# Kernel optimization log

Measured on AMD Instinct MI355X. Metric: run time of the kernel, lower is better.

## Reference

```python
import jax, jax.numpy as jnp
import numpy as np

B, D, E, K = 16384, 1024, 8, 2  # tokens, embed_size, experts, top-k
W_IMPORTANCE = 0.01


def setup_inputs() -> dict:
    key = jax.random.key(0)
    ks = jax.random.split(key, 8)
    s = 1.0 / np.sqrt(D)
    return {
        "x": jax.random.normal(ks[0], (B, D), dtype=jnp.float32),   # fused vision features
        "q": jax.random.normal(ks[1], (B, D), dtype=jnp.float32),   # text features
        # cross-attention (seq_len=1) collapses to V then output projection
        "Wv": jax.random.normal(ks[2], (D, D), dtype=jnp.float32) * s,
        "bv": jnp.zeros((D,), dtype=jnp.float32),
        "Wo": jax.random.normal(ks[3], (D, D), dtype=jnp.float32) * s,
        "bo": jnp.zeros((D,), dtype=jnp.float32),
        # gate linear
        "Wg": jax.random.normal(ks[4], (D, E), dtype=jnp.float32) * s,
        "bg": jnp.zeros((E,), dtype=jnp.float32),
        # experts: Linear -> SiLU -> Linear
        "W1": jax.random.normal(ks[5], (E, D, D), dtype=jnp.float32) * s,
        "b1": jnp.zeros((E, D), dtype=jnp.float32),
        "W2": jax.random.normal(ks[6], (E, D, D), dtype=jnp.float32) * s,
        "b2": jnp.zeros((E, D), dtype=jnp.float32),
    }


def reference(x, q, Wv, bv, Wo, bo, Wg, bg, W1, b1, W2, b2):
    # CrossAttention with q_len = kv_len = 1: softmax over a single key is 1,
    # so attention output = out_proj(V(q)).
    att = (q @ Wv + bv) @ Wo + bo                      # (B, D)
    gate_logits = att @ Wg + bg                        # (B, E)
    gate_prob = jax.nn.softmax(gate_logits, axis=-1)   # eval mode: no noise
    top_w, top_i = jax.lax.top_k(gate_prob, K)         # (B, K)
    top_w = jax.nn.softmax(top_w, axis=-1)             # renormalize over top-k

    y = jnp.zeros_like(x)
    for e in range(E):  # small fixed expert count
        w_e = jnp.sum(jnp.where(top_i == e, top_w, 0.0), axis=-1)  # (B,)
        h = jax.nn.silu(x @ W1[e] + b1[e]) @ W2[e] + b2[e]         # (B, D)
        y = y + w_e[:, None] * h

    importance = gate_prob.sum(axis=0)  # (E,)
    importance_loss = W_IMPORTANCE * (jnp.std(importance, ddof=1) / jnp.mean(importance)) ** 2
    return y, gate_prob, importance_loss
```

## Files before the change

kernel.cpp:

```cpp
#include <hip/hip_runtime.h>
#include <hip/hip_bf16.h>

#define Btok 16384
#define Ddim 1024
#define Eexp 8

typedef __attribute__((ext_vector_type(8))) short short8;
typedef __attribute__((ext_vector_type(4))) float f32x4;

__device__ inline unsigned short f2bf(float f) {
    unsigned int u = __float_as_uint(f);
    unsigned int r = (u + 0x7fffu + ((u >> 16) & 1u)) >> 16;
    return (unsigned short)r;
}

__device__ inline void gload16(const void* g, void* l) {
    __builtin_amdgcn_global_load_lds(
        (const __attribute__((address_space(1))) void*)g,
        (__attribute__((address_space(3))) void*)l, 16, 0, 0);
}

__global__ __launch_bounds__(256) void k_tmp(const float* __restrict__ Wo,
                                             const float* __restrict__ Wg,
                                             float* __restrict__ tmp) {
    int id = blockIdx.x * 256 + threadIdx.x;
    int d = id >> 3, e = id & 7;
    double s = 0.0;
    for (int k = 0; k < Ddim; ++k)
        s += (double)Wo[(long)d * Ddim + k] * (double)Wg[k * Eexp + e];
    tmp[id] = (float)s;
}

__global__ __launch_bounds__(256) void k_wc(const float* __restrict__ Wv,
                                            const float* __restrict__ tmp,
                                            float* __restrict__ WcT) {
    int id = blockIdx.x * 256 + threadIdx.x;
    int d = id >> 3, e = id & 7;
    double s = 0.0;
    for (int k = 0; k < Ddim; ++k)
        s += (double)Wv[(long)d * Ddim + k] * (double)tmp[k * Eexp + e];
    WcT[e * Ddim + d] = (float)s;
}

__global__ __launch_bounds__(512) void k_bc(const float* __restrict__ bv,
                                            const float* __restrict__ bo,
                                            const float* __restrict__ bg,
                                            const float* __restrict__ Wg,
                                            const float* __restrict__ tmp,
                                            float* __restrict__ bcomb) {
    int w = threadIdx.x >> 6, l = threadIdx.x & 63;
    double s = 0.0;
    for (int k = l; k < Ddim; k += 64)
        s += (double)bv[k] * (double)tmp[k * Eexp + w] +
             (double)bo[k] * (double)Wg[k * Eexp + w];
    #pragma unroll
    for (int off = 32; off; off >>= 1) s += __shfl_xor(s, off);
    if (l == 0) bcomb[w] = (float)s + bg[w];
}

__global__ __launch_bounds__(256) void k_convx(const float4* __restrict__ x,
                                               ushort4* __restrict__ xb) {
    int i = blockIdx.x * 256 + threadIdx.x;
    float4 v = x[i];
    ushort4 o;
    o.x = f2bf(v.x); o.y = f2bf(v.y); o.z = f2bf(v.z); o.w = f2bf(v.w);
    xb[i] = o;
}

__global__ __launch_bounds__(256) void k_convw(const float* __restrict__ W1,
                                               const float* __restrict__ W2,
                                               unsigned short* __restrict__ w1bT,
                                               unsigned short* __restrict__ w2bT) {
    __shared__ float tile[32][33];
    int bid = blockIdx.x;
    int arr = bid >> 13;
    int e = (bid >> 10) & 7, bi = (bid >> 5) & 31, bj = bid & 31;
    const float* src = (arr ? W2 : W1) + (long)e * Ddim * Ddim;
    unsigned short* dst = (arr ? w2bT : w1bT) + (long)e * Ddim * Ddim;
    int tr = threadIdx.x >> 5, tc = threadIdx.x & 31;
    #pragma unroll
    for (int i = 0; i < 4; ++i) {
        int dl = tr + i * 8;
        tile[dl][tc] = src[(long)(bi * 32 + dl) * Ddim + bj * 32 + tc];
    }
    __syncthreads();
    #pragma unroll
    for (int i = 0; i < 4; ++i) {
        int nl = tr + i * 8;
        dst[(long)(bj * 32 + nl) * Ddim + bi * 32 + tc] = f2bf(tile[tc][nl]);
    }
}

__global__ __launch_bounds__(256) void k_gate(const float* __restrict__ q,
                                              const float* __restrict__ WcT,
                                              const float* __restrict__ bcomb,
                                              float* __restrict__ gate_prob,
                                              int* __restrict__ choice,
                                              float2* __restrict__ w12,
                                              float* __restrict__ impP) {
    __shared__ float impL[4][8];
    int w = threadIdx.x >> 6, l = threadIdx.x & 63;
    int t = blockIdx.x * 4 + w;
    const float* qr = q + (long)t * Ddim;
    float acc[8] = {0, 0, 0, 0, 0, 0, 0, 0};
    #pragma unroll
    for (int i = 0; i < 4; ++i) {
        float4 qv = *(const float4*)(qr + (i * 64 + l) * 4);
        #pragma unroll
        for (int e = 0; e < 8; ++e) {
            float4 wv = *(const float4*)(WcT + e * Ddim + (i * 64 + l) * 4);
            acc[e] += qv.x * wv.x + qv.y * wv.y + qv.z * wv.z + qv.w * wv.w;
        }
    }
    #pragma unroll
    for (int off = 32; off; off >>= 1)
        #pragma unroll
        for (int e = 0; e < 8; ++e) acc[e] += __shfl_xor(acc[e], off);
    float lg[8], p[8];
    float m = -1e30f;
    #pragma unroll
    for (int e = 0; e < 8; ++e) { lg[e] = acc[e] + bcomb[e]; m = fmaxf(m, lg[e]); }
    float s = 0.f;
    #pragma unroll
    for (int e = 0; e < 8; ++e) { p[e] = expf(lg[e] - m); s += p[e]; }
    float inv = 1.f / s;
    #pragma unroll
    for (int e = 0; e < 8; ++e) p[e] *= inv;
    float p1 = -1.f, p2 = -1.f; int i1 = 0, i2 = 0;
    #pragma unroll
    for (int e = 0; e < 8; ++e) {
        float pe = p[e];
        if (pe > p1) { p2 = p1; i2 = i1; p1 = pe; i1 = e; }
        else if (pe > p2) { p2 = pe; i2 = e; }
    }
    float ee = expf(p2 - p1);
    float wa = 1.f / (1.f + ee);
    float wb = ee / (1.f + ee);
    if (l == 0) {
        #pragma unroll
        for (int e = 0; e < 8; ++e) gate_prob[(long)t * 8 + e] = p[e];
        #pragma unroll
        for (int e = 0; e < 8; ++e) impL[w][e] = p[e];
        choice[t] = i1 | (i2 << 8);
        w12[t] = make_float2(wa, wb);
    }
    __syncthreads();
    if (threadIdx.x < 8)
        impP[blockIdx.x * 8 + threadIdx.x] =
            impL[0][threadIdx.x] + impL[1][threadIdx.x] +
            impL[2][threadIdx.x] + impL[3][threadIdx.x];
}

__global__ __launch_bounds__(256) void k_route(const int* __restrict__ choice,
                                               const float2* __restrict__ w12,
                                               int* __restrict__ counts,
                                               int* __restrict__ tok,
                                               float* __restrict__ wgt) {
    __shared__ int cnt[8];
    __shared__ int base[8];
    if (threadIdx.x < 8) cnt[threadIdx.x] = 0;
    __syncthreads();
    int t = blockIdx.x * 256 + threadIdx.x;
    int ch = choice[t];
    int i1 = ch & 255, i2 = ch >> 8;
    float2 ww = w12[t];
    int lp1 = atomicAdd(&cnt[i1], 1);
    int lp2 = atomicAdd(&cnt[i2], 1);
    __syncthreads();
    if (threadIdx.x < 8)
        base[threadIdx.x] = atomicAdd(&counts[threadIdx.x], cnt[threadIdx.x]);
    __syncthreads();
    int p1 = base[i1] + lp1;
    tok[i1 * Btok + p1] = t; wgt[i1 * Btok + p1] = ww.x;
    int p2 = base[i2] + lp2;
    tok[i2 * Btok + p2] = t; wgt[i2 * Btok + p2] = ww.y;
}

template <int MODE>
__global__ __launch_bounds__(512) void k_gemm(const unsigned short* __restrict__ Abase,
                                              const unsigned short* __restrict__ WT,
                                              const float* __restrict__ bias,
                                              const int* __restrict__ counts,
                                              const int* __restrict__ tok,
                                              const float* __restrict__ wgt,
                                              unsigned short* __restrict__ Hout,
                                              float* __restrict__ y) {
    __shared__ __align__(16) char lds[131072];

    int bid = blockIdx.x;
    int wg = (bid & 7) * 256 + (bid >> 3);
    int ct = wg & 3, rt = (wg >> 2) & 63, e = wg >> 8;

    int n_e = counts[e];
    int r0 = rt * 256;
    if (r0 >= n_e) return;
    int off_e = 0;
    #pragma unroll
    for (int j = 0; j < 8; ++j) off_e += (j < e) ? counts[j] : 0;
    int n0 = ct * 256;

    int t = threadIdx.x;
    int w = t >> 6, l = t & 63;
    int wm = w >> 2, wn = w & 3;

    int tr = t >> 3;
    int sc = (t & 7) ^ (tr & 7);
    const char* srcA[4]; const char* srcB[4];
    #pragma unroll
    for (int ri = 0; ri < 4; ++ri) {
        int idx = r0 + ri * 64 + tr; if (idx > n_e - 1) idx = n_e - 1;
        long g = (MODE == 0) ? (long)tok[e * Btok + idx] : (long)(off_e + idx);
        srcA[ri] = (const char*)Abase + g * 2048 + sc * 16;
        srcB[ri] = (const char*)WT + ((long)e << 21) + (long)(n0 + ri * 64 + tr) * 2048 + sc * 16;
    }

    int rowAb = (wm * 128 + (l & 15)) * 128;
    int rowBb = (wn * 64 + (l & 15)) * 128;
    int x0 = (((l >> 4)) ^ (l & 7)) << 4;
    int x1 = (((l >> 4) + 4) ^ (l & 7)) << 4;

    f32x4 acc[8][4];
    #pragma unroll
    for (int mi = 0; mi < 8; ++mi)
        #pragma unroll
        for (int ni = 0; ni < 4; ++ni) acc[mi][ni] = {0.f, 0.f, 0.f, 0.f};

    auto stage = [&](int b) {
        char* ab = (char*)lds + b * 32768;
        char* bb = (char*)lds + 65536 + b * 32768;
        #pragma unroll
        for (int ri = 0; ri < 4; ++ri) {
            gload16(srcA[ri], ab + ri * 8192 + w * 1024);
            gload16(srcB[ri], bb + ri * 8192 + w * 1024);
            srcA[ri] += 128; srcB[ri] += 128;
        }
    };

    const int NT = Ddim / 64;
    stage(0);
    __syncthreads();
    int buf = 0;
    for (int kk = 0; kk < NT; ++kk) {
        if (kk + 1 < NT) stage(buf ^ 1);
        const char* Ap = (const char*)lds + buf * 32768;
        const char* Bp = (const char*)lds + 65536 + buf * 32768;
        #pragma unroll
        for (int ks = 0; ks < 2; ++ks) {
            int xo = ks ? x1 : x0;
            short8 av[8], bv[4];
            #pragma unroll
            for (int mi = 0; mi < 8; ++mi)
                av[mi] = *(const short8*)(Ap + rowAb + mi * 2048 + xo);
            #pragma unroll
            for (int ni = 0; ni < 4; ++ni)
                bv[ni] = *(const short8*)(Bp + rowBb + ni * 2048 + xo);
            #pragma unroll
            for (int mi = 0; mi < 8; ++mi)
                #pragma unroll
                for (int ni = 0; ni < 4; ++ni)
                    acc[mi][ni] = __builtin_amdgcn_mfma_f32_16x16x32_bf16(av[mi], bv[ni], acc[mi][ni], 0, 0, 0);
        }
        __syncthreads();
        buf ^= 1;
    }

    float bias4[4];
    #pragma unroll
    for (int ni = 0; ni < 4; ++ni)
        bias4[ni] = bias[e * Ddim + n0 + wn * 64 + ni * 16 + (l & 15)];

    #pragma unroll
    for (int mi = 0; mi < 8; ++mi) {
        #pragma unroll
        for (int j = 0; j < 4; ++j) {
            int rl = wm * 128 + mi * 16 + (l >> 4) * 4 + j;
            int r = r0 + rl;
            bool ok = r < n_e;
            int trow = 0; float wr = 0.f;
            if (MODE == 1) {
                int ri = ok ? r : 0;
                trow = tok[e * Btok + ri];
                wr = wgt[e * Btok + ri];
            }
            #pragma unroll
            for (int ni = 0; ni < 4; ++ni) {
                int col = n0 + wn * 64 + ni * 16 + (l & 15);
                float v = acc[mi][ni][j] + bias4[ni];
                if (MODE == 0) {
                    v = v / (1.f + __expf(-v));
                    if (ok) Hout[(long)(off_e + r) * Ddim + col] = f2bf(v);
                } else {
                    if (ok) atomicAdd(&y[(long)trow * Ddim + col], wr * v);
                }
            }
        }
    }
}

__global__ __launch_bounds__(256) void k_loss(const float* __restrict__ impP,
                                              float* __restrict__ out) {
    __shared__ float red[256];
    __shared__ float impF[8];
    for (int e = 0; e < 8; ++e) {
        float s = 0.f;
        for (int i = threadIdx.x; i < 4096; i += 256) s += impP[i * 8 + e];
        red[threadIdx.x] = s;
        __syncthreads();
        for (int st = 128; st > 0; st >>= 1) {
            if ((int)threadIdx.x < st) red[threadIdx.x] += red[threadIdx.x + st];
            __syncthreads();
        }
        if (threadIdx.x == 0) impF[e] = red[0];
        __syncthreads();
    }
    if (threadIdx.x == 0) {
        double mean = 0.0;
        for (int e = 0; e < 8; ++e) mean += (double)impF[e];
        mean /= 8.0;
        double var = 0.0;
        for (int e = 0; e < 8; ++e) {
            double d = (double)impF[e] - mean;
            var += d * d;
        }
        var /= 7.0;
        out[0] = (float)(0.01 * var / (mean * mean));
    }
}

extern "C" void kernel_launch(void* const* d_in, const int* in_sizes, int n_in,
                              void* d_out, int out_size, void* d_ws, size_t ws_size,
                              hipStream_t stream) {
    const float* x  = (const float*)d_in[0];
    const float* q  = (const float*)d_in[1];
    const float* Wv = (const float*)d_in[2];
    const float* bv = (const float*)d_in[3];
    const float* Wo = (const float*)d_in[4];
    const float* bo = (const float*)d_in[5];
    const float* Wg = (const float*)d_in[6];
    const float* bg = (const float*)d_in[7];
    const float* W1 = (const float*)d_in[8];
    const float* b1 = (const float*)d_in[9];
    const float* W2 = (const float*)d_in[10];
    const float* b2 = (const float*)d_in[11];

    float* y = (float*)d_out;
    float* gate_prob = y + (long)Btok * Ddim;
    float* loss = gate_prob + (long)Btok * Eexp;

    char* ws = (char*)d_ws;
    int*   counts = (int*)(ws + 0);
    float* bcomb  = (float*)(ws + 256);
    float* tmp    = (float*)(ws + 512);
    float* WcT    = (float*)(ws + 33280);
    float* impP   = (float*)(ws + 66048);
    int*   choice = (int*)(ws + 197120);
    float2* w12   = (float2*)(ws + 262656);
    int*   tok    = (int*)(ws + 393728);
    float* wgt    = (float*)(ws + 918016);
    unsigned short* xb   = (unsigned short*)(ws + 1442304);
    unsigned short* w1bT = (unsigned short*)(ws + 34996736);
    unsigned short* w2bT = (unsigned short*)(ws + 51773952);
    unsigned short* H    = (unsigned short*)(ws + 68551168);

    hipMemsetAsync(counts, 0, 32, stream);
    hipMemsetAsync(y, 0, (size_t)Btok * Ddim * sizeof(float), stream);

    k_tmp<<<32, 256, 0, stream>>>(Wo, Wg, tmp);
    k_wc <<<32, 256, 0, stream>>>(Wv, tmp, WcT);
    k_bc <<<1, 512, 0, stream>>>(bv, bo, bg, Wg, tmp, bcomb);
    k_convx<<<16384, 256, 0, stream>>>((const float4*)x, (ushort4*)xb);
    k_convw<<<16384, 256, 0, stream>>>(W1, W2, w1bT, w2bT);
    k_gate<<<4096, 256, 0, stream>>>(q, WcT, bcomb, gate_prob, choice, w12, impP);
    k_route<<<64, 256, 0, stream>>>(choice, w12, counts, tok, wgt);
    k_gemm<0><<<2048, 512, 0, stream>>>(xb, w1bT, b1, counts, tok, wgt, H, nullptr);
    k_gemm<1><<<2048, 512, 0, stream>>>(H, w2bT, b2, counts, tok, wgt, nullptr, y);
    k_loss<<<1, 256, 0, stream>>>(impP, loss);
}
```

Measured before the change: 507.4 us.

## Restructure expert GEMM into quadrant-interleaved pipeline with explicit waitcnt and barriers

```diff
diff --git a/kernel.cpp b/kernel.cpp
--- a/kernel.cpp
+++ b/kernel.cpp
@@ -19,6 +19,11 @@
         (const __attribute__((address_space(1))) void*)g,
         (__attribute__((address_space(3))) void*)l, 16, 0, 0);
 }
+
+#define MEMF() asm volatile("" ::: "memory")
+#define BARRIER() do { MEMF(); __builtin_amdgcn_s_barrier(); MEMF(); } while (0)
+#define VMW(n) do { asm volatile("s_waitcnt vmcnt(" #n ")" ::: "memory"); \
+                    __builtin_amdgcn_sched_barrier(0); } while (0)
 
 __global__ __launch_bounds__(256) void k_tmp(const float* __restrict__ Wo,
                                              const float* __restrict__ Wg,
@@ -186,6 +191,7 @@
                                               unsigned short* __restrict__ Hout,
                                               float* __restrict__ y) {
     __shared__ __align__(16) char lds[131072];
+    char* ldsp = (char*)lds;
 
     int bid = blockIdx.x;
     int wg = (bid & 7) * 256 + (bid >> 3);
@@ -201,7 +207,7 @@
 
     int t = threadIdx.x;
     int w = t >> 6, l = t & 63;
-    int wm = w >> 2, wn = w & 3;
+    int wqm = w >> 1, wqn = w & 1;
 
     int tr = t >> 3;
     int sc = (t & 7) ^ (tr & 7);
@@ -213,88 +219,144 @@
         srcA[ri] = (const char*)Abase + g * 2048 + sc * 16;
         srcB[ri] = (const char*)WT + ((long)e << 21) + (long)(n0 + ri * 64 + tr) * 2048 + sc * 16;
     }
-
-    int rowAb = (wm * 128 + (l & 15)) * 128;
-    int rowBb = (wn * 64 + (l & 15)) * 128;
-    int x0 = (((l >> 4)) ^ (l & 7)) << 4;
+    int dstoff = tr * 128 + (t & 7) * 16;
+
+    int rA = (wqm * 32 + (l & 15)) * 128;
+    int rB = (wqn * 64 + (l & 15)) * 128;
+    int x0 = ((l >> 4) ^ (l & 7)) << 4;
     int x1 = (((l >> 4) + 4) ^ (l & 7)) << 4;
 
-    f32x4 acc[8][4];
-    #pragma unroll
-    for (int mi = 0; mi < 8; ++mi)
-        #pragma unroll
-        for (int ni = 0; ni < 4; ++ni) acc[mi][ni] = {0.f, 0.f, 0.f, 0.f};
-
-    auto stage = [&](int b) {
-        char* ab = (char*)lds + b * 32768;
-        char* bb = (char*)lds + 65536 + b * 32768;
-        #pragma unroll
-        for (int ri = 0; ri < 4; ++ri) {
-            gload16(srcA[ri], ab + ri * 8192 + w * 1024);
-            gload16(srcB[ri], bb + ri * 8192 + w * 1024);
-            srcA[ri] += 128; srcB[ri] += 128;
-        }
-    };
+    f32x4 acc[2][2][2][4];
+    #pragma unroll
+    for (int qa = 0; qa < 2; ++qa)
+        #pragma unroll
+        for (int qb = 0; qb < 2; ++qb)
+            #pragma unroll
+            for (int mi = 0; mi < 2; ++mi)
+                #pragma unroll
+                for (int ni = 0; ni < 4; ++ni) acc[qa][qb][mi][ni] = {0.f, 0.f, 0.f, 0.f};
+
+    short8 av[2][2], bv[4][2];
+
+#define STAGE_A(h, nb) do { \
+        char* d_ = ldsp + (nb) * 32768 + (h) * 16384 + dstoff; \
+        gload16(srcA[2*(h)], d_); gload16(srcA[2*(h)+1], d_ + 8192); \
+        srcA[2*(h)] += 128; srcA[2*(h)+1] += 128; } while (0)
+#define STAGE_B(h, nb) do { \
+        char* d_ = ldsp + 65536 + (nb) * 32768 + (h) * 16384 + dstoff; \
+        gload16(srcB[2*(h)], d_); gload16(srcB[2*(h)+1], d_ + 8192); \
+        srcB[2*(h)] += 128; srcB[2*(h)+1] += 128; } while (0)
+#define READ_AV(qa, c) do { \
+        const char* p_ = ldsp + (c) * 32768 + (qa) * 16384 + rA; \
+        av[0][0] = *(const short8*)(p_ + x0);        av[0][1] = *(const short8*)(p_ + x1); \
+        av[1][0] = *(const short8*)(p_ + 2048 + x0); av[1][1] = *(const short8*)(p_ + 2048 + x1); } while (0)
+#define READ_BV(qb, c) do { \
+        const char* p_ = ldsp + 65536 + (c) * 32768 + (qb) * 16384 + rB; \
+        _Pragma("unroll") \
+        for (int ni_ = 0; ni_ < 4; ++ni_) { \
+            bv[ni_][0] = *(const short8*)(p_ + ni_ * 2048 + x0); \
+            bv[ni_][1] = *(const short8*)(p_ + ni_ * 2048 + x1); } } while (0)
+#define MFMA16(qa, qb) do { \
+        __builtin_amdgcn_s_setprio(1); \
+        _Pragma("unroll") \
+        for (int mi_ = 0; mi_ < 2; ++mi_) \
+            _Pragma("unroll") \
+            for (int ni_ = 0; ni_ < 4; ++ni_) { \
+                acc[qa][qb][mi_][ni_] = __builtin_amdgcn_mfma_f32_16x16x32_bf16(av[mi_][0], bv[ni_][0], acc[qa][qb][mi_][ni_], 0, 0, 0); \
+                acc[qa][qb][mi_][ni_] = __builtin_amdgcn_mfma_f32_16x16x32_bf16(av[mi_][1], bv[ni_][1], acc[qa][qb][mi_][ni_], 0, 0, 0); } \
+        __builtin_amdgcn_s_setprio(0); \
+        __builtin_amdgcn_sched_barrier(0); } while (0)
 
     const int NT = Ddim / 64;
-    stage(0);
-    __syncthreads();
-    int buf = 0;
-    for (int kk = 0; kk < NT; ++kk) {
-        if (kk + 1 < NT) stage(buf ^ 1);
-        const char* Ap = (const char*)lds + buf * 32768;
-        const char* Bp = (const char*)lds + 65536 + buf * 32768;
-        #pragma unroll
-        for (int ks = 0; ks < 2; ++ks) {
-            int xo = ks ? x1 : x0;
-            short8 av[8], bv[4];
+    STAGE_A(0, 0); STAGE_B(0, 0); STAGE_A(1, 0); STAGE_B(1, 0);
+    VMW(4); BARRIER();
+
+    for (int kt = 0; kt < NT - 1; ++kt) {
+        int c = kt & 1, nb = c ^ 1;
+        READ_AV(0, c); READ_BV(0, c);
+        STAGE_A(0, nb);
+        BARRIER();
+        MFMA16(0, 0);
+        VMW(4); BARRIER();
+        READ_AV(1, c);
+        STAGE_B(0, nb);
+        BARRIER();
+        MFMA16(1, 0);
+        VMW(4); BARRIER();
+        READ_BV(1, c);
+        STAGE_A(1, nb);
+        BARRIER();
+        MFMA16(1, 1);
+        BARRIER();
+        READ_AV(0, c);
+        STAGE_B(1, nb);
+        BARRIER();
+        MFMA16(0, 1);
+        VMW(4); BARRIER();
+    }
+    {
+        const int c = (NT - 1) & 1;
+        READ_AV(0, c); READ_BV(0, c);
+        BARRIER();
+        MFMA16(0, 0);
+        VMW(2); BARRIER();
+        READ_AV(1, c);
+        BARRIER();
+        MFMA16(1, 0);
+        VMW(0); BARRIER();
+        READ_BV(1, c);
+        BARRIER();
+        MFMA16(1, 1);
+        BARRIER();
+        READ_AV(0, c);
+        BARRIER();
+        MFMA16(0, 1);
+    }
+
+    float bias8[2][4];
+    #pragma unroll
+    for (int qb = 0; qb < 2; ++qb)
+        #pragma unroll
+        for (int ni = 0; ni < 4; ++ni)
+            bias8[qb][ni] = bias[e * Ddim + n0 + qb * 128 + wqn * 64 + ni * 16 + (l & 15)];
+
+    #pragma unroll
+    for (int qa = 0; qa < 2; ++qa) {
+        #pragma unroll
+        for (int mi = 0; mi < 2; ++mi) {
             #pragma unroll
-            for (int mi = 0; mi < 8; ++mi)
-                av[mi] = *(const short8*)(Ap + rowAb + mi * 2048 + xo);
-            #pragma unroll
-            for (int ni = 0; ni < 4; ++ni)
-                bv[ni] = *(const short8*)(Bp + rowBb + ni * 2048 + xo);
-            #pragma unroll
-            for (int mi = 0; mi < 8; ++mi)
+            for (int j = 0; j < 4; ++j) {
+                int rl = qa * 128 + wqm * 32 + mi * 16 + (l >> 4) * 4 + j;
+                int r = r0 + rl;
+                bool ok = r < n_e;
+                int trow = 0; float wr = 0.f;
+                if (MODE == 1) {
+                    int ri = ok ? r : 0;
+                    trow = tok[e * Btok + ri];
+                    wr = wgt[e * Btok + ri];
+                }
                 #pragma unroll
-                for (int ni = 0; ni < 4; ++ni)
-                    acc[mi][ni] = __builtin_amdgcn_mfma_f32_16x16x32_bf16(av[mi], bv[ni], acc[mi][ni], 0, 0, 0);
-        }
-        __syncthreads();
-        buf ^= 1;
-    }
-
-    float bias4[4];
-    #pragma unroll
-    for (int ni = 0; ni < 4; ++ni)
-        bias4[ni] = bias[e * Ddim + n0 + wn * 64 + ni * 16 + (l & 15)];
-
-    #pragma unroll
-    for (int mi = 0; mi < 8; ++mi) {
-        #pragma unroll
-        for (int j = 0; j < 4; ++j) {
-            int rl = wm * 128 + mi * 16 + (l >> 4) * 4 + j;
-            int r = r0 + rl;
-            bool ok = r < n_e;
-            int trow = 0; float wr = 0.f;
-            if (MODE == 1) {
-                int ri = ok ? r : 0;
-                trow = tok[e * Btok + ri];
-                wr = wgt[e * Btok + ri];
-            }
-            #pragma unroll
-            for (int ni = 0; ni < 4; ++ni) {
-                int col = n0 + wn * 64 + ni * 16 + (l & 15);
-                float v = acc[mi][ni][j] + bias4[ni];
-                if (MODE == 0) {
-                    v = v / (1.f + __expf(-v));
-                    if (ok) Hout[(long)(off_e + r) * Ddim + col] = f2bf(v);
-                } else {
-                    if (ok) atomicAdd(&y[(long)trow * Ddim + col], wr * v);
+                for (int qb = 0; qb < 2; ++qb) {
+                    #pragma unroll
+                    for (int ni = 0; ni < 4; ++ni) {
+                        int col = n0 + qb * 128 + wqn * 64 + ni * 16 + (l & 15);
+                        float v = acc[qa][qb][mi][ni][j] + bias8[qb][ni];
+                        if (MODE == 0) {
+                            v = v / (1.f + __expf(-v));
+                            if (ok) Hout[(long)(off_e + r) * Ddim + col] = f2bf(v);
+                        } else {
+                            if (ok) atomicAdd(&y[(long)trow * Ddim + col], wr * v);
+                        }
+                    }
                 }
             }
         }
     }
+#undef STAGE_A
+#undef STAGE_B
+#undef READ_AV
+#undef READ_BV
+#undef MFMA16
 }
 
 __global__ __launch_bounds__(256) void k_loss(const float* __restrict__ impP,
```

Measured after the change: 510.9 us. About the same (+0.7%).

## Shrink expert GEMM tiles to 128x128 with 256 threads and single-buffered LDS

Applied to the files above, without the earlier changes.

```diff
diff --git a/kernel.cpp b/kernel.cpp
--- a/kernel.cpp
+++ b/kernel.cpp
@@ -177,91 +177,83 @@
 }
 
 template <int MODE>
-__global__ __launch_bounds__(512) void k_gemm(const unsigned short* __restrict__ Abase,
-                                              const unsigned short* __restrict__ WT,
-                                              const float* __restrict__ bias,
-                                              const int* __restrict__ counts,
-                                              const int* __restrict__ tok,
-                                              const float* __restrict__ wgt,
-                                              unsigned short* __restrict__ Hout,
-                                              float* __restrict__ y) {
-    __shared__ __align__(16) char lds[131072];
+__global__ __launch_bounds__(256, 4) void k_gemm(const unsigned short* __restrict__ Abase,
+                                                 const unsigned short* __restrict__ WT,
+                                                 const float* __restrict__ bias,
+                                                 const int* __restrict__ counts,
+                                                 const int* __restrict__ tok,
+                                                 const float* __restrict__ wgt,
+                                                 unsigned short* __restrict__ Hout,
+                                                 float* __restrict__ y) {
+    __shared__ __align__(16) char lds[32768];
+    char* ldsp = (char*)lds;
 
     int bid = blockIdx.x;
-    int wg = (bid & 7) * 256 + (bid >> 3);
-    int ct = wg & 3, rt = (wg >> 2) & 63, e = wg >> 8;
+    int e = bid & 7;
+    int k = bid >> 3;
+    int rt = k >> 3, ct = k & 7;
 
     int n_e = counts[e];
-    int r0 = rt * 256;
+    int r0 = rt * 128;
     if (r0 >= n_e) return;
     int off_e = 0;
     #pragma unroll
     for (int j = 0; j < 8; ++j) off_e += (j < e) ? counts[j] : 0;
-    int n0 = ct * 256;
+    int n0 = ct * 128;
 
     int t = threadIdx.x;
     int w = t >> 6, l = t & 63;
-    int wm = w >> 2, wn = w & 3;
+    int wm = w >> 1, wn = w & 1;
 
     int tr = t >> 3;
     int sc = (t & 7) ^ (tr & 7);
     const char* srcA[4]; const char* srcB[4];
     #pragma unroll
     for (int ri = 0; ri < 4; ++ri) {
-        int idx = r0 + ri * 64 + tr; if (idx > n_e - 1) idx = n_e - 1;
+        int idx = r0 + ri * 32 + tr; if (idx > n_e - 1) idx = n_e - 1;
         long g = (MODE == 0) ? (long)tok[e * Btok + idx] : (long)(off_e + idx);
         srcA[ri] = (const char*)Abase + g * 2048 + sc * 16;
-        srcB[ri] = (const char*)WT + ((long)e << 21) + (long)(n0 + ri * 64 + tr) * 2048 + sc * 16;
-    }
-
-    int rowAb = (wm * 128 + (l & 15)) * 128;
-    int rowBb = (wn * 64 + (l & 15)) * 128;
-    int x0 = (((l >> 4)) ^ (l & 7)) << 4;
+        srcB[ri] = (const char*)WT + ((long)e << 21) + (long)(n0 + ri * 32 + tr) * 2048 + sc * 16;
+    }
+    int dstoff = tr * 128 + (t & 7) * 16;
+
+    int rA = (wm * 64 + (l & 15)) * 128;
+    int rB = (wn * 64 + (l & 15)) * 128;
+    int x0 = ((l >> 4) ^ (l & 7)) << 4;
     int x1 = (((l >> 4) + 4) ^ (l & 7)) << 4;
 
-    f32x4 acc[8][4];
-    #pragma unroll
-    for (int mi = 0; mi < 8; ++mi)
+    f32x4 acc[4][4];
+    #pragma unroll
+    for (int mi = 0; mi < 4; ++mi)
         #pragma unroll
         for (int ni = 0; ni < 4; ++ni) acc[mi][ni] = {0.f, 0.f, 0.f, 0.f};
 
-    auto stage = [&](int b) {
-        char* ab = (char*)lds + b * 32768;
-        char* bb = (char*)lds + 65536 + b * 32768;
+    const int NT = Ddim / 64;
+    for (int kk = 0; kk < NT; ++kk) {
         #pragma unroll
         for (int ri = 0; ri < 4; ++ri) {
-            gload16(srcA[ri], ab + ri * 8192 + w * 1024);
-            gload16(srcB[ri], bb + ri * 8192 + w * 1024);
+            gload16(srcA[ri], ldsp + ri * 4096 + dstoff);
+            gload16(srcB[ri], ldsp + 16384 + ri * 4096 + dstoff);
             srcA[ri] += 128; srcB[ri] += 128;
         }
-    };
-
-    const int NT = Ddim / 64;
-    stage(0);
-    __syncthreads();
-    int buf = 0;
-    for (int kk = 0; kk < NT; ++kk) {
-        if (kk + 1 < NT) stage(buf ^ 1);
-        const char* Ap = (const char*)lds + buf * 32768;
-        const char* Bp = (const char*)lds + 65536 + buf * 32768;
+        __syncthreads();
         #pragma unroll
         for (int ks = 0; ks < 2; ++ks) {
             int xo = ks ? x1 : x0;
-            short8 av[8], bv[4];
+            short8 av[4], bv[4];
             #pragma unroll
-            for (int mi = 0; mi < 8; ++mi)
-                av[mi] = *(const short8*)(Ap + rowAb + mi * 2048 + xo);
+            for (int mi = 0; mi < 4; ++mi)
+                av[mi] = *(const short8*)(ldsp + rA + mi * 2048 + xo);
             #pragma unroll
             for (int ni = 0; ni < 4; ++ni)
-                bv[ni] = *(const short8*)(Bp + rowBb + ni * 2048 + xo);
+                bv[ni] = *(const short8*)(ldsp + 16384 + rB + ni * 2048 + xo);
             #pragma unroll
-            for (int mi = 0; mi < 8; ++mi)
+            for (int mi = 0; mi < 4; ++mi)
                 #pragma unroll
                 for (int ni = 0; ni < 4; ++ni)
                     acc[mi][ni] = __builtin_amdgcn_mfma_f32_16x16x32_bf16(av[mi], bv[ni], acc[mi][ni], 0, 0, 0);
         }
         __syncthreads();
-        buf ^= 1;
     }
 
     float bias4[4];
@@ -270,10 +262,10 @@
         bias4[ni] = bias[e * Ddim + n0 + wn * 64 + ni * 16 + (l & 15)];
 
     #pragma unroll
-    for (int mi = 0; mi < 8; ++mi) {
+    for (int mi = 0; mi < 4; ++mi) {
         #pragma unroll
         for (int j = 0; j < 4; ++j) {
-            int rl = wm * 128 + mi * 16 + (l >> 4) * 4 + j;
+            int rl = wm * 64 + mi * 16 + (l >> 4) * 4 + j;
             int r = r0 + rl;
             bool ok = r < n_e;
             int trow = 0; float wr = 0.f;
@@ -372,7 +364,7 @@
     k_convw<<<16384, 256, 0, stream>>>(W1, W2, w1bT, w2bT);
     k_gate<<<4096, 256, 0, stream>>>(q, WcT, bcomb, gate_prob, choice, w12, impP);
     k_route<<<64, 256, 0, stream>>>(choice, w12, counts, tok, wgt);
-    k_gemm<0><<<2048, 512, 0, stream>>>(xb, w1bT, b1, counts, tok, wgt, H, nullptr);
-    k_gemm<1><<<2048, 512, 0, stream>>>(H, w2bT, b2, counts, tok, wgt, nullptr, y);
+    k_gemm<0><<<4096, 256, 0, stream>>>(xb, w1bT, b1, counts, tok, wgt, H, nullptr);
+    k_gemm<1><<<4096, 256, 0, stream>>>(H, w2bT, b2, counts, tok, wgt, nullptr, y);
     k_loss<<<1, 256, 0, stream>>>(impP, loss);
 }
```

New measurement: 454.4 us. -10.4%, faster.
